# Kernel tuning notes

Measured on AMD Instinct MI355X. Metric: run time of the kernel, lower is better.

Reference implementation:

```python
import jax, jax.numpy as jnp
import numpy as np


def _shift(w):
    # max(0, -min(w)): scalar shift making w + shift non-negative
    return jnp.maximum(0.0, -jnp.min(w))


def shifted_linear(x, W, b=None):
    # F.linear with non-negative weights plus row-sum correction
    alpha = _shift(W)
    y = x @ (W + alpha).T - alpha * jnp.sum(x, axis=-1, keepdims=True)
    if b is not None:
        y = y + b
    return y


def shifted_depthwise_conv(x, w, b):
    # x: (B, D, L), w: (D, 1, K) depthwise; causal-style padding K-1, sliced to L by caller
    alpha = _shift(w)
    k = w.shape[2]
    pad = k - 1
    dn = ('NCH', 'OIH', 'NCH')
    groups = w.shape[0]
    y = jax.lax.conv_general_dilated(x, w + alpha, (1,), [(pad, pad)],
                                     dimension_numbers=dn, feature_group_count=groups)
    ones_k = jnp.ones_like(w)
    ssum = jax.lax.conv_general_dilated(x, ones_k, (1,), [(pad, pad)],
                                        dimension_numbers=dn, feature_group_count=groups)
    return y - alpha * ssum + b[None, :, None]


def setup_inputs() -> dict:
    key = jax.random.key(0)
    ks = jax.random.split(key, 10)
    d_model, d_inner, d_state, d_conv, dt_rank = 1024, 2048, 16, 4, 64
    B, L = 2, 1024
    s = 0.05
    return {
        'hidden_states': jax.random.normal(ks[0], (B, L, d_model), jnp.float32),
        'W_in': jax.random.normal(ks[1], (2 * d_inner, d_model), jnp.float32) * s,
        'conv_w': jax.random.normal(ks[2], (d_inner, 1, d_conv), jnp.float32) * 0.3,
        'conv_b': jax.random.normal(ks[3], (d_inner,), jnp.float32) * s,
        'W_x': jax.random.normal(ks[4], (dt_rank + 2 * d_state, d_inner), jnp.float32) * s,
        'W_dt': jax.random.normal(ks[5], (d_inner, dt_rank), jnp.float32) * s,
        'dt_bias': jax.random.normal(ks[6], (d_inner,), jnp.float32),
        'W_out': jax.random.normal(ks[7], (d_model, d_inner), jnp.float32) * s,
        'A_log': jax.random.normal(ks[8], (d_inner, d_state), jnp.float32) * 0.5,
        'D': jax.random.normal(ks[9], (d_inner,), jnp.float32),
    }


def reference(hidden_states, W_in, conv_w, conv_b, W_x, W_dt, dt_bias, W_out, A_log, D):
    b, l, dm = hidden_states.shape
    d_inner = conv_w.shape[0]
    d_state = A_log.shape[1]
    dt_rank = W_dt.shape[1]

    A = jnp.exp(A_log)  # (d_inner, d_state), always positive

    # in_proj over (b*l, d_model) -> (b, 2*d_inner, l)
    xz = shifted_linear(hidden_states.reshape(b * l, dm), W_in)
    xz = xz.reshape(b, l, 2 * d_inner).transpose(0, 2, 1)
    x, z = xz[:, :d_inner], xz[:, d_inner:]

    # depthwise shifted conv + SiLU activation, truncated to seqlen
    x = jax.nn.silu(shifted_depthwise_conv(x, conv_w, conv_b)[..., :l])

    # x_proj -> dt_raw, B, C
    x_dbl = shifted_linear(x.transpose(0, 2, 1).reshape(b * l, d_inner), W_x)
    dt_raw = x_dbl[:, :dt_rank]
    Bm = x_dbl[:, dt_rank:dt_rank + d_state].reshape(b, l, d_state).transpose(0, 2, 1)  # (b,n,l)
    Cm = x_dbl[:, dt_rank + d_state:].reshape(b, l, d_state).transpose(0, 2, 1)         # (b,n,l)
    dt = shifted_linear(dt_raw, W_dt).reshape(b, l, d_inner).transpose(0, 2, 1)          # (b,d,l)

    # delta activation (softplus) with bias, clamped
    delta = jnp.clip(jax.nn.softplus(dt + dt_bias[None, :, None]), 1e-4, 20.0)

    # global scalar shifts for B and C
    beta = _shift(Bm)
    gamma = _shift(Cm)
    B_nn = Bm + beta
    C_nn = Cm + gamma

    # precomputed per-step operands, scan axis first: (l, b, d, n)
    deltaA = jnp.exp(-jnp.einsum('bdl,dn->lbdn', delta, A))
    dBu = jnp.einsum('bdl,bnl,bdl->lbdn', delta, B_nn, x)
    C_scan = C_nn.transpose(2, 0, 1)  # (l, b, n)

    def step(xc, inp):
        dA_i, dBu_i, C_i = inp
        xc = dA_i * xc + dBu_i                                   # (b,d,n)
        y = jnp.einsum('bdn,bn->bd', xc, C_i) - gamma * jnp.sum(xc, axis=-1)
        return xc, y

    x0 = jnp.zeros((b, d_inner, d_state), dtype=delta.dtype)
    _, ys = jax.lax.scan(step, x0, (deltaA, dBu, C_scan))        # ys: (l, b, d)

    y = ys.transpose(1, 2, 0) + x * D[None, :, None]             # (b, d, l) skip term
    y = y * jax.nn.silu(z)                                       # gate activation

    out = shifted_linear(y.transpose(0, 2, 1).reshape(b * l, d_inner), W_out)
    return out.reshape(b, l, dm)
```

## Files before the change

kernel.cpp:

```cpp
#include <hip/hip_runtime.h>
#include <math.h>

#define DM 1024
#define DI 2048
#define DS 16
#define DTR 64
#define NB 2
#define LL 1024
#define TT (NB*LL)
#define SCH 32
#define NCH (LL/SCH)

typedef unsigned short u16;
typedef __attribute__((ext_vector_type(8))) short bf16x8;
typedef __attribute__((ext_vector_type(4))) float f32x4;

#define LOG2E 1.4426950408889634f

__device__ inline u16 f2bf(float f) {
  union { float f; unsigned u; } c; c.f = f;
  unsigned u = c.u;
  return (u16)((u + 0x7fffu + ((u >> 16) & 1u)) >> 16);
}
__device__ inline float bf2f(u16 u) {
  union { unsigned u; float f; } c; c.u = ((unsigned)u) << 16;
  return c.f;
}

__device__ inline unsigned fkey(float f) {
  union { float f; unsigned u; } c; c.f = f;
  return (c.u & 0x80000000u) ? ~c.u : (c.u | 0x80000000u);
}
__device__ inline float funkey(unsigned k) {
  union { unsigned u; float f; } c;
  c.u = (k & 0x80000000u) ? (k & 0x7fffffffu) : ~k;
  return c.f;
}

__device__ inline bf16x8 cvt8(float4 a, float4 b) {
  bf16x8 w;
  w[0] = (short)f2bf(a.x); w[1] = (short)f2bf(a.y);
  w[2] = (short)f2bf(a.z); w[3] = (short)f2bf(a.w);
  w[4] = (short)f2bf(b.x); w[5] = (short)f2bf(b.y);
  w[6] = (short)f2bf(b.z); w[7] = (short)f2bf(b.w);
  return w;
}

#define GLDS16(g, l) __builtin_amdgcn_global_load_lds( \
    (const __attribute__((address_space(1))) unsigned int*)(g), \
    (__attribute__((address_space(3))) unsigned int*)(l), 16, 0, 0)

template<int BM, int BN, int EPI, int OB, int CGd, int ASRC, int BMIN>
__global__ __launch_bounds__(256) void gemm_k(
    const void* __restrict__ Av, const u16* __restrict__ B,
    void* __restrict__ Cv, int M, int N, int K, int lda, int ldb, int kpb,
    const float* __restrict__ bias,
    const float* __restrict__ minsrc, unsigned* __restrict__ betakey) {
  constexpr int WAVES_M = BM / 64;
  constexpr int WAVES_N = 4 / WAVES_M;
  constexpr int WTM = 4;
  constexpr int WTN = BN / (WAVES_N * 16);
  constexpr int ASLABS = BM / 16;
  constexpr int SLABS = (BM + BN) / 16;
  constexpr int SPW = SLABS / 4;
  __shared__ u16 As[BM * 32];
  __shared__ u16 Bs[BN * 32];
  __shared__ float sm4[4];
  const int tid = threadIdx.x;
  const int wave = tid >> 6;
  const int lane = tid & 63;
  const int bm = blockIdx.y * BM;
  const int bn = blockIdx.x * BN;
  const int wm = (wave / WAVES_N) * 64;
  const int wn = (wave % WAVES_N) * (WTN * 16);
  const int r4 = lane >> 2;
  const int kc = (lane & 3) * 8;
  const int fr = lane & 15;
  const int fq = lane >> 4;
  const int koff = blockIdx.z * kpb;
  float* C = (float*)Cv;
  u16* C16 = (u16*)Cv;

  if constexpr (BMIN == 1) {
    int fb = blockIdx.y * gridDim.x + blockIdx.x;
    if (fb < 64) {
      const int t0 = fb * 32;
      float mn = 3.4e38f;
      for (int i = tid; i < 32 * 16; i += 256) {
        int t = t0 + (i >> 4), n = i & 15;
        mn = fminf(mn, minsrc[t * 96 + 64 + n]);
      }
#pragma unroll
      for (int o = 32; o; o >>= 1) mn = fminf(mn, __shfl_down(mn, o));
      if ((tid & 63) == 0) sm4[tid >> 6] = mn;
      __syncthreads();
      if (tid == 0)
        atomicMin(betakey, fkey(fminf(fminf(sm4[0], sm4[1]), fminf(sm4[2], sm4[3]))));
      __syncthreads();
    }
  }

  f32x4 acc[WTM][WTN];
#pragma unroll
  for (int i = 0; i < WTM; ++i)
#pragma unroll
    for (int j = 0; j < WTN; ++j) acc[i][j] = (f32x4){0.f, 0.f, 0.f, 0.f};

  for (int k0 = koff; k0 < koff + kpb; k0 += 32) {
#pragma unroll
    for (int s = wave * SPW; s < (wave + 1) * SPW; ++s) {
      if (s < ASLABS) {
        int row = s * 16 + r4;
        if constexpr (ASRC == 0) {
          GLDS16((const u16*)Av + (size_t)(bm + row) * lda + k0 + kc, &As[s * 512]);
        } else {
          const float* src = (const float*)Av + (size_t)(bm + row) * lda + k0 + kc;
          float4 v0 = *(const float4*)src;
          float4 v1 = *(const float4*)(src + 4);
          *(bf16x8*)&As[s * 512 + lane * 8] = cvt8(v0, v1);
        }
      } else {
        int bs = s - ASLABS;
        int row = bs * 16 + r4;
        GLDS16(B + (size_t)(bn + row) * ldb + k0 + kc, &Bs[bs * 512]);
      }
    }
    __syncthreads();
    bf16x8 af[WTM], bf[WTN];
#pragma unroll
    for (int i = 0; i < WTM; ++i)
      af[i] = *(const bf16x8*)&As[(wm + 16 * i + fr) * 32 + fq * 8];
#pragma unroll
    for (int j = 0; j < WTN; ++j)
      bf[j] = *(const bf16x8*)&Bs[(wn + 16 * j + fr) * 32 + fq * 8];
#pragma unroll
    for (int i = 0; i < WTM; ++i)
#pragma unroll
      for (int j = 0; j < WTN; ++j)
        acc[i][j] = __builtin_amdgcn_mfma_f32_16x16x32_bf16(af[i], bf[j], acc[i][j], 0, 0, 0);
    __syncthreads();
  }

#pragma unroll
  for (int i = 0; i < WTM; ++i) {
    int row0 = bm + wm + 16 * i + fq * 4;
#pragma unroll
    for (int j = 0; j < WTN; ++j) {
      int col = bn + wn + 16 * j + fr;
#pragma unroll
      for (int r = 0; r < 4; ++r) {
        float v = acc[i][j][r];
        if (EPI == 1) {
          v += bias[col];
          float sp = (v > 20.0f) ? v : log1pf(expf(v));
          v = fminf(fmaxf(sp, 1e-4f), 20.0f);
        }
        if (OB == 1) {
          C16[(size_t)(row0 + r) * N + col] = f2bf(v);
        } else {
          if (CGd == 0 || col < CGd) {
            const int ldc = (CGd > 0) ? CGd : N;
            atomicAdd(&C[(size_t)(row0 + r) * ldc + col], v);
          }
        }
      }
    }
  }
}

__global__ __launch_bounds__(256) void cast_all(
    const float* __restrict__ hs, const float* __restrict__ win,
    const float* __restrict__ wout, const float* __restrict__ wx,
    const float* __restrict__ wdt,
    u16* __restrict__ hs_bf, u16* __restrict__ win_bf,
    u16* __restrict__ wout_bf, u16* __restrict__ wx_bf,
    u16* __restrict__ wdt_bf, float* __restrict__ xdb,
    float* __restrict__ outz, unsigned* __restrict__ betakey) {
  int gid = blockIdx.x * 256 + threadIdx.x;
  if (gid == 0) betakey[0] = 0xFFFFFFFFu;
  const float* src; u16* dst; int off;
  if (gid < 524288)       { src = hs;   dst = hs_bf;   off = gid; }
  else if (gid < 1572864) { src = win;  dst = win_bf;  off = gid - 524288; }
  else if (gid < 2097152) { src = wout; dst = wout_bf; off = gid - 1572864; }
  else if (gid < 2146304) { src = wx;   dst = wx_bf;   off = gid - 2097152; }
  else if (gid < 2179072) { src = wdt;  dst = wdt_bf;  off = gid - 2146304; }
  else if (gid < 2195456) {
    ushort4 z4 = {0, 0, 0, 0};
    ((ushort4*)wx_bf)[49152 + gid - 2179072] = z4;
    return;
  } else if (gid < 2244608) {
    float4 z = {0.f, 0.f, 0.f, 0.f};
    ((float4*)xdb)[gid - 2195456] = z;
    return;
  } else {
    float4 z = {0.f, 0.f, 0.f, 0.f};
    ((float4*)outz)[gid - 2244608] = z;
    return;
  }
  float4 v = ((const float4*)src)[off];
  ushort4 o;
  o.x = f2bf(v.x); o.y = f2bf(v.y); o.z = f2bf(v.z); o.w = f2bf(v.w);
  ((ushort4*)dst)[off] = o;
}

__global__ __launch_bounds__(256) void conv_silu4(
    const u16* __restrict__ xz, const float* __restrict__ w,
    const float* __restrict__ cb, u16* __restrict__ xc_bf) {
  int gid = blockIdx.x * 256 + threadIdx.x;
  int dq = (gid & 511) * 4;
  int t = gid >> 9;
  int l = t & (LL - 1);
  float wv[4][4];
#pragma unroll
  for (int j = 0; j < 4; ++j) {
    float4 ww = *(const float4*)&w[(dq + j) * 4];
    wv[j][0] = ww.x; wv[j][1] = ww.y; wv[j][2] = ww.z; wv[j][3] = ww.w;
  }
  float4 acc = *(const float4*)&cb[dq];
#pragma unroll
  for (int k = 0; k < 4; ++k) {
    int ll = l - 3 + k;
    if (ll < 0) continue;
    ushort4 xv = *(const ushort4*)&xz[(size_t)(t - 3 + k) * (2 * DI) + dq];
    acc.x += bf2f(xv.x) * wv[0][k]; acc.y += bf2f(xv.y) * wv[1][k];
    acc.z += bf2f(xv.z) * wv[2][k]; acc.w += bf2f(xv.w) * wv[3][k];
  }
  acc.x /= (1.0f + expf(-acc.x)); acc.y /= (1.0f + expf(-acc.y));
  acc.z /= (1.0f + expf(-acc.z)); acc.w /= (1.0f + expf(-acc.w));
  ushort4 o;
  o.x = f2bf(acc.x); o.y = f2bf(acc.y); o.z = f2bf(acc.z); o.w = f2bf(acc.w);
  *(ushort4*)&xc_bf[(size_t)t * DI + dq] = o;
}

__global__ __launch_bounds__(256) void scan_pass1(
    const u16* __restrict__ delta, const u16* __restrict__ xc_bf,
    const float* __restrict__ xdb, const float* __restrict__ A_log,
    const unsigned* __restrict__ betak,
    float* __restrict__ hend, float* __restrict__ Ssum) {
  const int d = blockIdx.x * 256 + threadIdx.x;
  const int c = blockIdx.y;
  const int b = blockIdx.z;
  __shared__ float Bsh[SCH][16];
  const float beta = fmaxf(0.0f, -funkey(betak[0]));
  const int t0 = b * LL + c * SCH;
  for (int i = threadIdx.x; i < SCH * 16; i += 256) {
    int tt = i >> 4, n = i & 15;
    Bsh[tt][n] = xdb[(size_t)(t0 + tt) * 96 + 64 + n] + beta;
  }
  __syncthreads();
  float Av2[16];
#pragma unroll
  for (int n = 0; n < 16; ++n) Av2[n] = expf(A_log[d * 16 + n]) * LOG2E;
  float h[16];
#pragma unroll
  for (int n = 0; n < 16; ++n) h[n] = 0.f;
  float S = 0.f;
  for (int tt = 0; tt < SCH; ++tt) {
    int t = t0 + tt;
    float dv = bf2f(delta[(size_t)t * DI + d]);
    float xv = bf2f(xc_bf[(size_t)t * DI + d]);
    float dx = dv * xv;
    S += dv;
#pragma unroll
    for (int n = 0; n < 16; ++n) {
      float a = __builtin_amdgcn_exp2f(-dv * Av2[n]);
      h[n] = a * h[n] + dx * Bsh[tt][n];
    }
  }
  size_t base = (((size_t)(b * NCH + c) * DI) + d) * 16;
#pragma unroll
  for (int n = 0; n < 16; ++n) hend[base + n] = h[n];
  Ssum[((size_t)(b * NCH + c) * DI) + d] = S;
}

__global__ __launch_bounds__(256) void scan_pass2(
    float* __restrict__ hend, const float* __restrict__ Ssum,
    const float* __restrict__ A_log) {
  int gid = blockIdx.x * 256 + threadIdx.x;
  int n = gid & 15;
  int d = (gid >> 4) & (DI - 1);
  int b = gid >> 15;
  float Av2 = expf(A_log[d * 16 + n]) * LOG2E;
  float H = 0.f;
  for (int c = 0; c < NCH; ++c) {
    size_t cb = ((size_t)(b * NCH + c) * DI) + d;
    float hl = hend[cb * 16 + n];
    float p = __builtin_amdgcn_exp2f(-Av2 * Ssum[cb]);
    hend[cb * 16 + n] = H;
    H = p * H + hl;
  }
}

__global__ __launch_bounds__(256) void scan_pass3(
    const u16* __restrict__ delta, const u16* __restrict__ xc_bf,
    const float* __restrict__ xdb, const u16* __restrict__ xz_bf,
    const float* __restrict__ A_log, const float* __restrict__ Dp,
    const unsigned* __restrict__ betak, const float* __restrict__ hstart,
    u16* __restrict__ ybf) {
  const int d = blockIdx.x * 256 + threadIdx.x;
  const int c = blockIdx.y;
  const int b = blockIdx.z;
  __shared__ float Bsh[SCH][16];
  __shared__ float Csh[SCH][16];
  const float beta = fmaxf(0.0f, -funkey(betak[0]));
  const int t0 = b * LL + c * SCH;
  for (int i = threadIdx.x; i < SCH * 16; i += 256) {
    int tt = i >> 4, n = i & 15;
    size_t row = (size_t)(t0 + tt) * 96;
    Bsh[tt][n] = xdb[row + 64 + n] + beta;
    Csh[tt][n] = xdb[row + 80 + n];
  }
  __syncthreads();
  float Av2[16];
#pragma unroll
  for (int n = 0; n < 16; ++n) Av2[n] = expf(A_log[d * 16 + n]) * LOG2E;
  float h[16];
  size_t base = (((size_t)(b * NCH + c) * DI) + d) * 16;
#pragma unroll
  for (int n = 0; n < 16; ++n) h[n] = hstart[base + n];
  const float Dd = Dp[d];
  for (int tt = 0; tt < SCH; ++tt) {
    int t = t0 + tt;
    float dv = bf2f(delta[(size_t)t * DI + d]);
    float xv = bf2f(xc_bf[(size_t)t * DI + d]);
    float dx = dv * xv;
    float yv = 0.f;
#pragma unroll
    for (int n = 0; n < 16; ++n) {
      float a = __builtin_amdgcn_exp2f(-dv * Av2[n]);
      h[n] = a * h[n] + dx * Bsh[tt][n];
      yv += h[n] * Csh[tt][n];
    }
    float zv = bf2f(xz_bf[(size_t)t * (2 * DI) + DI + d]);
    float out = (yv + xv * Dd) * (zv / (1.0f + expf(-zv)));
    ybf[(size_t)t * DI + d] = f2bf(out);
  }
}

extern "C" void kernel_launch(void* const* d_in, const int* in_sizes, int n_in,
                              void* d_out, int out_size, void* d_ws, size_t ws_size,
                              hipStream_t stream) {
  const float* hs      = (const float*)d_in[0];
  const float* W_in    = (const float*)d_in[1];
  const float* conv_w  = (const float*)d_in[2];
  const float* conv_b  = (const float*)d_in[3];
  const float* W_x     = (const float*)d_in[4];
  const float* W_dt    = (const float*)d_in[5];
  const float* dt_bias = (const float*)d_in[6];
  const float* W_out   = (const float*)d_in[7];
  const float* A_log   = (const float*)d_in[8];
  const float* Dp      = (const float*)d_in[9];
  float* out = (float*)d_out;

  float* ws       = (float*)d_ws;
  float* xz_bfR   = ws;
  float* xcv_bfR  = xz_bfR + (size_t)TT * 2 * DI / 2;
  float* xdb      = xcv_bfR + (size_t)TT * DI / 2;
  float* dlt_bfR  = xdb + (size_t)TT * 96;
  float* betab    = dlt_bfR + (size_t)TT * DI / 2;
  float* hend     = betab + 64;
  float* Ssum     = hend + (size_t)NB * NCH * DI * 16;
  float* hs_bfR   = Ssum + (size_t)NB * NCH * DI;
  float* win_bfR  = hs_bfR + (size_t)TT * DM / 2;
  float* wout_bfR = win_bfR + (size_t)2 * DI * DM / 2;
  float* wx_bfR   = wout_bfR + (size_t)DM * DI / 2;
  float* wdt_bfR  = wx_bfR + 131072;

  u16* xz_bf   = (u16*)xz_bfR;
  u16* xcv_bf  = (u16*)xcv_bfR;
  u16* dlt_bf  = (u16*)dlt_bfR;
  u16* hs_bf   = (u16*)hs_bfR;
  u16* win_bf  = (u16*)win_bfR;
  u16* wout_bf = (u16*)wout_bfR;
  u16* wx_bf   = (u16*)wx_bfR;
  u16* wdt_bf  = (u16*)wdt_bfR;
  unsigned* betakey = (unsigned*)betab;
  u16* ybf     = (u16*)win_bfR;

  dim3 blk(256);

  cast_all<<<10816, blk, 0, stream>>>(hs, W_in, W_out, W_x, W_dt,
                                      hs_bf, win_bf, wout_bf, wx_bf, wdt_bf,
                                      xdb, out, betakey);

  gemm_k<128, 128, 0, 1, 0, 0, 0>
      <<<dim3(4096 / 128, TT / 128), blk, 0, stream>>>(
      hs_bf, win_bf, xz_bf, TT, 2 * DI, DM, DM, DM, DM,
      nullptr, nullptr, nullptr);

  conv_silu4<<<(TT * DI / 4) / 256, blk, 0, stream>>>(xz_bf, conv_w, conv_b, xcv_bf);

  gemm_k<64, 128, 0, 2, 96, 0, 0>
      <<<dim3(1, TT / 64, 8), blk, 0, stream>>>(
      xcv_bf, wx_bf, xdb, TT, 128, DI, DI, DI, DI / 8,
      nullptr, nullptr, nullptr);

  gemm_k<64, 128, 1, 1, 0, 1, 1>
      <<<dim3(DI / 128, TT / 64), blk, 0, stream>>>(
      xdb, wdt_bf, dlt_bf, TT, DI, DTR, 96, DTR, DTR,
      dt_bias, xdb, betakey);

  scan_pass1<<<dim3(DI / 256, NCH, NB), blk, 0, stream>>>(
      dlt_bf, xcv_bf, xdb, A_log, betakey, hend, Ssum);
  scan_pass2<<<(NB * DI * DS) / 256, blk, 0, stream>>>(hend, Ssum, A_log);
  scan_pass3<<<dim3(DI / 256, NCH, NB), blk, 0, stream>>>(
      dlt_bf, xcv_bf, xdb, xz_bf, A_log, Dp, betakey, hend, ybf);

  gemm_k<128, 128, 0, 2, 0, 0, 0>
      <<<dim3(DM / 128, TT / 128, 4), blk, 0, stream>>>(
      ybf, wout_bf, out, TT, DM, DI, DI, DI, DI / 4,
      nullptr, nullptr, nullptr);
}
```

Measured before the change: 263.4 us.

## Double-buffer GEMM shared-memory tiles and switch transcendentals to fast hardware intrinsics

The GEMM kernel now keeps two shared-memory buffers. It issues the global-to-LDS loads for the next K tile before computing MFMAs on the current one, and waits with an explicit waitcnt plus barrier instead of two __syncthreads per iteration. Separately, expf, log1pf and the division-based SiLU are replaced with exp2/log/rcp hardware intrinsics in the softplus epilogue, conv SiLU, scan A-coefficient setup and output gating. Both aim to cut latency and instruction cost. The price is twice the LDS use, which may lower occupancy, and slightly less accurate math.

```diff
diff --git a/kernel.cpp b/kernel.cpp
--- a/kernel.cpp
+++ b/kernel.cpp
@@ -16,6 +16,7 @@
 typedef __attribute__((ext_vector_type(4))) float f32x4;
 
 #define LOG2E 1.4426950408889634f
+#define LN2   0.6931471805599453f
 
 __device__ inline u16 f2bf(float f) {
   union { float f; unsigned u; } c; c.f = f;
@@ -25,6 +26,10 @@
 __device__ inline float bf2f(u16 u) {
   union { unsigned u; float f; } c; c.u = ((unsigned)u) << 16;
   return c.f;
+}
+
+__device__ inline float fsilu(float x) {
+  return x * __builtin_amdgcn_rcpf(1.0f + __builtin_amdgcn_exp2f(-x * LOG2E));
 }
 
 __device__ inline unsigned fkey(float f) {
@@ -63,8 +68,8 @@
   constexpr int ASLABS = BM / 16;
   constexpr int SLABS = (BM + BN) / 16;
   constexpr int SPW = SLABS / 4;
-  __shared__ u16 As[BM * 32];
-  __shared__ u16 Bs[BN * 32];
+  __shared__ u16 As[2][BM * 32];
+  __shared__ u16 Bs[2][BN * 32];
   __shared__ float sm4[4];
   const int tid = threadIdx.x;
   const int wave = tid >> 6;
@@ -100,45 +105,57 @@
     }
   }
 
-  f32x4 acc[WTM][WTN];
-#pragma unroll
-  for (int i = 0; i < WTM; ++i)
-#pragma unroll
-    for (int j = 0; j < WTN; ++j) acc[i][j] = (f32x4){0.f, 0.f, 0.f, 0.f};
-
-  for (int k0 = koff; k0 < koff + kpb; k0 += 32) {
+  auto stage = [&](int k0, int bufi) {
 #pragma unroll
     for (int s = wave * SPW; s < (wave + 1) * SPW; ++s) {
       if (s < ASLABS) {
         int row = s * 16 + r4;
         if constexpr (ASRC == 0) {
-          GLDS16((const u16*)Av + (size_t)(bm + row) * lda + k0 + kc, &As[s * 512]);
+          GLDS16((const u16*)Av + (size_t)(bm + row) * lda + k0 + kc,
+                 &As[bufi][s * 512]);
         } else {
           const float* src = (const float*)Av + (size_t)(bm + row) * lda + k0 + kc;
           float4 v0 = *(const float4*)src;
           float4 v1 = *(const float4*)(src + 4);
-          *(bf16x8*)&As[s * 512 + lane * 8] = cvt8(v0, v1);
+          *(bf16x8*)&As[bufi][s * 512 + lane * 8] = cvt8(v0, v1);
         }
       } else {
         int bs = s - ASLABS;
         int row = bs * 16 + r4;
-        GLDS16(B + (size_t)(bn + row) * ldb + k0 + kc, &Bs[bs * 512]);
+        GLDS16(B + (size_t)(bn + row) * ldb + k0 + kc, &Bs[bufi][bs * 512]);
       }
     }
-    __syncthreads();
+  };
+
+  f32x4 acc[WTM][WTN];
+#pragma unroll
+  for (int i = 0; i < WTM; ++i)
+#pragma unroll
+    for (int j = 0; j < WTN; ++j) acc[i][j] = (f32x4){0.f, 0.f, 0.f, 0.f};
+
+  const int NT = kpb >> 5;
+  stage(koff, 0);
+  asm volatile("s_waitcnt vmcnt(0) lgkmcnt(0)" ::: "memory");
+  __builtin_amdgcn_s_barrier();
+  for (int t = 0; t < NT; ++t) {
+    const int cur = t & 1;
+    if (t + 1 < NT) stage(koff + (t + 1) * 32, cur ^ 1);
     bf16x8 af[WTM], bf[WTN];
 #pragma unroll
     for (int i = 0; i < WTM; ++i)
-      af[i] = *(const bf16x8*)&As[(wm + 16 * i + fr) * 32 + fq * 8];
+      af[i] = *(const bf16x8*)&As[cur][(wm + 16 * i + fr) * 32 + fq * 8];
 #pragma unroll
     for (int j = 0; j < WTN; ++j)
-      bf[j] = *(const bf16x8*)&Bs[(wn + 16 * j + fr) * 32 + fq * 8];
+      bf[j] = *(const bf16x8*)&Bs[cur][(wn + 16 * j + fr) * 32 + fq * 8];
 #pragma unroll
     for (int i = 0; i < WTM; ++i)
 #pragma unroll
       for (int j = 0; j < WTN; ++j)
         acc[i][j] = __builtin_amdgcn_mfma_f32_16x16x32_bf16(af[i], bf[j], acc[i][j], 0, 0, 0);
-    __syncthreads();
+    if (t + 1 < NT) {
+      asm volatile("s_waitcnt vmcnt(0) lgkmcnt(0)" ::: "memory");
+      __builtin_amdgcn_s_barrier();
+    }
   }
 
 #pragma unroll
@@ -152,7 +169,9 @@
         float v = acc[i][j][r];
         if (EPI == 1) {
           v += bias[col];
-          float sp = (v > 20.0f) ? v : log1pf(expf(v));
+          float sp;
+          if (v > 20.0f) sp = v;
+          else sp = __builtin_amdgcn_logf(1.0f + __builtin_amdgcn_exp2f(v * LOG2E)) * LN2;
           v = fminf(fmaxf(sp, 1e-4f), 20.0f);
         }
         if (OB == 1) {
@@ -225,8 +244,8 @@
     acc.x += bf2f(xv.x) * wv[0][k]; acc.y += bf2f(xv.y) * wv[1][k];
     acc.z += bf2f(xv.z) * wv[2][k]; acc.w += bf2f(xv.w) * wv[3][k];
   }
-  acc.x /= (1.0f + expf(-acc.x)); acc.y /= (1.0f + expf(-acc.y));
-  acc.z /= (1.0f + expf(-acc.z)); acc.w /= (1.0f + expf(-acc.w));
+  acc.x = fsilu(acc.x); acc.y = fsilu(acc.y);
+  acc.z = fsilu(acc.z); acc.w = fsilu(acc.w);
   ushort4 o;
   o.x = f2bf(acc.x); o.y = f2bf(acc.y); o.z = f2bf(acc.z); o.w = f2bf(acc.w);
   *(ushort4*)&xc_bf[(size_t)t * DI + dq] = o;
@@ -250,7 +269,8 @@
   __syncthreads();
   float Av2[16];
 #pragma unroll
-  for (int n = 0; n < 16; ++n) Av2[n] = expf(A_log[d * 16 + n]) * LOG2E;
+  for (int n = 0; n < 16; ++n)
+    Av2[n] = __builtin_amdgcn_exp2f(A_log[d * 16 + n] * LOG2E) * LOG2E;
   float h[16];
 #pragma unroll
   for (int n = 0; n < 16; ++n) h[n] = 0.f;
@@ -280,7 +300,7 @@
   int n = gid & 15;
   int d = (gid >> 4) & (DI - 1);
   int b = gid >> 15;
-  float Av2 = expf(A_log[d * 16 + n]) * LOG2E;
+  float Av2 = __builtin_amdgcn_exp2f(A_log[d * 16 + n] * LOG2E) * LOG2E;
   float H = 0.f;
   for (int c = 0; c < NCH; ++c) {
     size_t cb = ((size_t)(b * NCH + c) * DI) + d;
@@ -313,7 +333,8 @@
   __syncthreads();
   float Av2[16];
 #pragma unroll
-  for (int n = 0; n < 16; ++n) Av2[n] = expf(A_log[d * 16 + n]) * LOG2E;
+  for (int n = 0; n < 16; ++n)
+    Av2[n] = __builtin_amdgcn_exp2f(A_log[d * 16 + n] * LOG2E) * LOG2E;
   float h[16];
   size_t base = (((size_t)(b * NCH + c) * DI) + d) * 16;
 #pragma unroll
@@ -332,7 +353,7 @@
       yv += h[n] * Csh[tt][n];
     }
     float zv = bf2f(xz_bf[(size_t)t * (2 * DI) + DI + d]);
-    float out = (yv + xv * Dd) * (zv / (1.0f + expf(-zv)));
+    float out = (yv + xv * Dd) * fsilu(zv);
     ybf[(size_t)t * DI + d] = f2bf(out);
   }
 }
```

Measured after the change: 239.0 us. 9.3% less time.
